# Kernel tuning notes

Hardware: AMD Instinct MI355X
Metric: run time of the kernel (lower is better)

Reference implementation:

```python
import jax, jax.numpy as jnp
import numpy as np

NEG_INF = -1e9


def setup_inputs() -> dict:
    key = jax.random.key(0)
    ks = jax.random.split(key, 9)
    B, T, E, D, H = 64, 2048, 1024, 1024, 1024
    enc = jax.random.normal(ks[0], (B, T, E), dtype=jnp.float32)
    dec = jax.random.normal(ks[1], (B, D), dtype=jnp.float32)
    inp_mask = jax.random.randint(ks[2], (B, T), 0, 2, dtype=jnp.int32)
    s = 1.0 / np.sqrt(H)
    W_enc = jax.random.normal(ks[3], (E, H), dtype=jnp.float32) * s
    b_enc = jax.random.normal(ks[4], (H,), dtype=jnp.float32) * 0.01
    W_dec = jax.random.normal(ks[5], (D, H), dtype=jnp.float32) * s
    b_dec = jax.random.normal(ks[6], (H,), dtype=jnp.float32) * 0.01
    W_out = jax.random.normal(ks[7], (H, 1), dtype=jnp.float32) * s
    b_out = jax.random.normal(ks[8], (1,), dtype=jnp.float32) * 0.01
    return {"enc": enc, "dec": dec, "inp_mask": inp_mask,
            "W_enc": W_enc, "b_enc": b_enc, "W_dec": W_dec, "b_dec": b_dec,
            "W_out": W_out, "b_out": b_out}


def reference(enc, dec, inp_mask, W_enc, b_enc, W_dec, b_dec, W_out, b_out):
    # a: [B, T, H] = Linear(enc) + Linear(dec)[:, None, :]
    a = jnp.einsum('bte,eh->bth', enc, W_enc) + b_enc \
        + (dec @ W_dec + b_dec)[:, None, :]
    a = jnp.tanh(a)
    # scores: [B, T]
    scores = (jnp.einsum('bth,h->bt', a, W_out[:, 0]) + b_out[0])
    scores = jnp.where(inp_mask == 0, NEG_INF, scores)
    probs = jax.nn.softmax(scores, axis=1)            # [B, T]
    attn = jnp.einsum('bt,bte->be', probs, enc)       # [B, E]
    return (attn, probs)
```

## Files before the change

### kernel.cpp

```cpp
#include <hip/hip_runtime.h>
#include <hip/hip_bf16.h>

typedef __attribute__((ext_vector_type(4))) float f32x4;
typedef __attribute__((ext_vector_type(4))) unsigned int u32x4;
typedef __attribute__((ext_vector_type(8))) short s16x8;

static constexpr int Bb = 64;
static constexpr int Tt = 2048;
static constexpr int Ee = 1024;
static constexpr int Hh = 1024;
static constexpr int ATTN_N = Bb * Ee;
static constexpr int PROB_N = Bb * Tt;

__device__ inline unsigned short f2bf(float f) {
    __hip_bfloat16 h = __float2bfloat16(f);
    return __builtin_bit_cast(unsigned short, h);
}

__device__ inline void gload_lds16(const unsigned short* g, unsigned short* l) {
    __builtin_amdgcn_global_load_lds(
        (const __attribute__((address_space(1))) void*)g,
        (__attribute__((address_space(3))) void*)l,
        16, 0, 0);
}

__global__ void wtrans_kernel(const float* __restrict__ w_enc,
                              unsigned short* __restrict__ w16t) {
    __shared__ float tile[32][33];
    const int bx = blockIdx.x & 31;
    const int by = blockIdx.x >> 5;
    const int tx = threadIdx.x & 31;
    const int ty = threadIdx.x >> 5;
#pragma unroll
    for (int j = 0; j < 4; ++j) {
        int e = by * 32 + ty + j * 8;
        int h = bx * 32 + tx;
        tile[ty + j * 8][tx] = w_enc[e * Hh + h];
    }
    __syncthreads();
#pragma unroll
    for (int j = 0; j < 4; ++j) {
        int h = bx * 32 + ty + j * 8;
        int e = by * 32 + tx;
        w16t[h * Ee + e] = f2bf(tile[tx][ty + j * 8]);
    }
}

__global__ void ddec_kernel(const float* __restrict__ dec,
                            const float* __restrict__ w_dec,
                            const float* __restrict__ b_dec,
                            const float* __restrict__ b_enc,
                            float* __restrict__ ddec) {
    const int b = blockIdx.y;
    const int h = blockIdx.x * 256 + threadIdx.x;
    float acc = b_dec[h] + b_enc[h];
    const float* dr = dec + b * Ee;
#pragma unroll 4
    for (int e = 0; e < Ee; ++e) {
        acc += dr[e] * w_dec[e * Hh + h];
    }
    ddec[b * Hh + h] = acc;
}

__global__ __launch_bounds__(512, 2) void gemm_score_kernel(
    const float* __restrict__ enc, const unsigned short* __restrict__ w16t,
    const float* __restrict__ ddec, const float* __restrict__ w_out,
    float* __restrict__ scores) {
    __shared__ unsigned short As[2][256 * 32];
    __shared__ unsigned short Bs[2][256 * 32];

    const int tid = threadIdx.x;
    const int lane = tid & 63;
    const int wid = tid >> 6;
    const int wm = wid >> 2;
    const int wn = wid & 3;
    const int lr = lane & 15;
    const int lg = lane >> 4;

    const int g = blockIdx.x;
    const int xcd = g & 7;
    const int slot = g >> 3;
    const int ntile = slot & 3;
    const int mtile = xcd * 64 + (slot >> 2);
    const int m0 = mtile * 256;
    const int n0 = ntile * 256;
    const int bidx = m0 >> 11;

    const int ar = tid >> 2;
    const int as = tid & 3;

    f32x4 rs[4];

    auto loadA = [&](int kt) {
        const float* src = enc + (size_t)(m0 + ar) * Ee + kt * 32 + as * 8;
#pragma unroll
        for (int ci = 0; ci < 2; ++ci) {
            rs[ci * 2]     = *reinterpret_cast<const f32x4*>(src + (size_t)(128 * ci) * Ee);
            rs[ci * 2 + 1] = *reinterpret_cast<const f32x4*>(src + (size_t)(128 * ci) * Ee + 4);
        }
    };
    auto writeA = [&](int db) {
        char* abase = (char*)&As[db][0];
#pragma unroll
        for (int ci = 0; ci < 2; ++ci) {
            int r = ar + 128 * ci;
            int xr = (r & 3) ^ ((r >> 2) & 1);
            u32x4 w;
            w.x = (unsigned)f2bf(rs[2 * ci].x) | ((unsigned)f2bf(rs[2 * ci].y) << 16);
            w.y = (unsigned)f2bf(rs[2 * ci].z) | ((unsigned)f2bf(rs[2 * ci].w) << 16);
            w.z = (unsigned)f2bf(rs[2 * ci + 1].x) | ((unsigned)f2bf(rs[2 * ci + 1].y) << 16);
            w.w = (unsigned)f2bf(rs[2 * ci + 1].z) | ((unsigned)f2bf(rs[2 * ci + 1].w) << 16);
            *reinterpret_cast<u32x4*>(abase + r * 64 + ((as ^ xr) << 4)) = w;
        }
    };
    auto stageB = [&](int kt, int db) {
        const int sg = (lane & 3) ^ ((lane >> 2) & 3) ^ ((lane >> 4) & 1);
#pragma unroll
        for (int c = 0; c < 2; ++c) {
            int rr = (wid * 2 + c) * 16 + (lane >> 2);
            const unsigned short* src = w16t + (size_t)(n0 + rr) * Ee + kt * 32 + sg * 8;
            gload_lds16(src, &Bs[db][(wid * 2 + c) * 512]);
        }
    };

    f32x4 acc[8][4];
#pragma unroll
    for (int ni = 0; ni < 4; ++ni) {
        float dv = ddec[bidx * Hh + n0 + wn * 64 + ni * 16 + lr];
#pragma unroll
        for (int mi = 0; mi < 8; ++mi) {
            acc[mi][ni].x = dv; acc[mi][ni].y = dv;
            acc[mi][ni].z = dv; acc[mi][ni].w = dv;
        }
    }

    u32x4 af[4], bf[4];
    auto readB4 = [&](int db) {
        const char* bbase = (const char*)&Bs[db][0];
#pragma unroll
        for (int ni = 0; ni < 4; ++ni) {
            int r = wn * 64 + ni * 16 + lr;
            int xr = (r & 3) ^ ((r >> 2) & 1);
            bf[ni] = *reinterpret_cast<const u32x4*>(
                bbase + r * 64 + ((lg ^ xr) << 4));
        }
    };
    auto readA4 = [&](int db, int mib) {
        const char* abase = (const char*)&As[db][0];
#pragma unroll
        for (int k = 0; k < 4; ++k) {
            int r = wm * 128 + (mib + k) * 16 + lr;
            int xr = (r & 3) ^ ((r >> 2) & 1);
            af[k] = *reinterpret_cast<const u32x4*>(
                abase + r * 64 + ((lg ^ xr) << 4));
        }
    };
    auto mfma16 = [&](int mib) {
        __builtin_amdgcn_s_setprio(1);
#pragma unroll
        for (int k = 0; k < 4; ++k)
#pragma unroll
            for (int ni = 0; ni < 4; ++ni)
                acc[mib + k][ni] = __builtin_amdgcn_mfma_f32_16x16x32_bf16(
                    __builtin_bit_cast(s16x8, af[k]),
                    __builtin_bit_cast(s16x8, bf[ni]),
                    acc[mib + k][ni], 0, 0, 0);
        __builtin_amdgcn_s_setprio(0);
    };

#define LGKM0() asm volatile("s_waitcnt lgkmcnt(0)" ::: "memory")

    loadA(0);
    writeA(0);
    LGKM0();
    stageB(0, 0);
    loadA(1);
    asm volatile("s_waitcnt vmcnt(4)" ::: "memory");
    __builtin_amdgcn_s_barrier();

#pragma unroll 1
    for (int tt = 0; tt < 32; tt += 2) {
#pragma unroll
        for (int pp = 0; pp < 2; ++pp) {
            const int t = tt + pp;
            if (t < 31) stageB(t + 1, pp ^ 1);
            readB4(pp);
            readA4(pp, 0);
            mfma16(0);
            if (t < 31) writeA(pp ^ 1);
            readA4(pp, 4);
            mfma16(4);
            LGKM0();
            if (t < 30) {
                loadA(t + 2);
                asm volatile("s_waitcnt vmcnt(4)" ::: "memory");
            } else if (t == 30) {
                asm volatile("s_waitcnt vmcnt(0)" ::: "memory");
            }
            __builtin_amdgcn_s_barrier();
        }
    }

    float wout[4];
#pragma unroll
    for (int ni = 0; ni < 4; ++ni)
        wout[ni] = w_out[n0 + wn * 64 + ni * 16 + lr];

#pragma unroll
    for (int mi = 0; mi < 8; ++mi) {
#pragma unroll
        for (int i = 0; i < 4; ++i) {
            float s = 0.f;
#pragma unroll
            for (int ni = 0; ni < 4; ++ni) {
                float x = (i == 0) ? acc[mi][ni].x : (i == 1) ? acc[mi][ni].y
                           : (i == 2) ? acc[mi][ni].z : acc[mi][ni].w;
                float t = 1.f - 2.f / (__expf(2.f * x) + 1.f);
                s += t * wout[ni];
            }
            s += __shfl_xor(s, 1);
            s += __shfl_xor(s, 2);
            s += __shfl_xor(s, 4);
            s += __shfl_xor(s, 8);
            if (lr == 0) {
                int row = m0 + wm * 128 + mi * 16 + 4 * lg + i;
                atomicAdd(&scores[row], s);
            }
        }
    }
#undef LGKM0
}

__global__ __launch_bounds__(256) void softmax_kernel(float* __restrict__ sc,
                                                      const int* __restrict__ mask) {
    __shared__ float red[256];
    const int b = blockIdx.x;
    const int tid = threadIdx.x;
    float* row = sc + b * Tt;
    const int* mrow = mask + b * Tt;

    float v[8];
    float mx = -3.0e38f;
#pragma unroll
    for (int j = 0; j < 8; ++j) {
        int t = tid + j * 256;
        float s = row[t];
        v[j] = (mrow[t] == 0) ? -1.0e9f : s;
        mx = fmaxf(mx, v[j]);
    }
    red[tid] = mx;
    __syncthreads();
    for (int off = 128; off > 0; off >>= 1) {
        if (tid < off) red[tid] = fmaxf(red[tid], red[tid + off]);
        __syncthreads();
    }
    mx = red[0];
    __syncthreads();

    float p[8];
    float sum = 0.f;
#pragma unroll
    for (int j = 0; j < 8; ++j) {
        p[j] = __expf(v[j] - mx);
        sum += p[j];
    }
    red[tid] = sum;
    __syncthreads();
    for (int off = 128; off > 0; off >>= 1) {
        if (tid < off) red[tid] += red[tid + off];
        __syncthreads();
    }
    float inv = 1.f / red[0];
#pragma unroll
    for (int j = 0; j < 8; ++j)
        row[tid + j * 256] = p[j] * inv;
}

__global__ __launch_bounds__(256) void attn_kernel(const float* __restrict__ enc,
                                                   const float* __restrict__ probs,
                                                   float* __restrict__ attn) {
    __shared__ float pr[128];
    const int b = blockIdx.y;
    const int tc = blockIdx.x;
    const int tid = threadIdx.x;
    if (tid < 128) pr[tid] = probs[b * Tt + tc * 128 + tid];
    __syncthreads();

    const int e0 = tid * 4;
    f32x4 acc; acc.x = 0.f; acc.y = 0.f; acc.z = 0.f; acc.w = 0.f;
    const float* base = enc + (size_t)b * Tt * Ee + (size_t)tc * 128 * Ee + e0;
#pragma unroll 4
    for (int t = 0; t < 128; ++t) {
        f32x4 vv = *reinterpret_cast<const f32x4*>(base + (size_t)t * Ee);
        float pw = pr[t];
        acc.x += pw * vv.x; acc.y += pw * vv.y;
        acc.z += pw * vv.z; acc.w += pw * vv.w;
    }
    atomicAdd(&attn[b * Ee + e0 + 0], acc.x);
    atomicAdd(&attn[b * Ee + e0 + 1], acc.y);
    atomicAdd(&attn[b * Ee + e0 + 2], acc.z);
    atomicAdd(&attn[b * Ee + e0 + 3], acc.w);
}

extern "C" void kernel_launch(void* const* d_in, const int* in_sizes, int n_in,
                              void* d_out, int out_size, void* d_ws, size_t ws_size,
                              hipStream_t stream) {
    const float* enc      = (const float*)d_in[0];
    const float* dec      = (const float*)d_in[1];
    const int*   inp_mask = (const int*)d_in[2];
    const float* W_enc    = (const float*)d_in[3];
    const float* b_enc    = (const float*)d_in[4];
    const float* W_dec    = (const float*)d_in[5];
    const float* b_dec    = (const float*)d_in[6];
    const float* W_out    = (const float*)d_in[7];

    float* attn   = (float*)d_out;
    float* scores = (float*)d_out + ATTN_N;

    unsigned short* w16t = (unsigned short*)d_ws;
    float* ddec = attn;

    hipMemsetAsync(scores, 0, (size_t)PROB_N * sizeof(float), stream);

    wtrans_kernel<<<dim3(1024), 256, 0, stream>>>(W_enc, w16t);
    ddec_kernel<<<dim3(4, 64), 256, 0, stream>>>(dec, W_dec, b_dec, b_enc, ddec);
    gemm_score_kernel<<<dim3(2048), 512, 0, stream>>>(enc, w16t, ddec, W_out, scores);

    hipMemsetAsync(attn, 0, (size_t)ATTN_N * sizeof(float), stream);

    softmax_kernel<<<dim3(64), 256, 0, stream>>>(scores, inp_mask);
    attn_kernel<<<dim3(16, 64), 256, 0, stream>>>(enc, scores, attn);
}
```

Baseline: 650.8 us.

## Emit bf16 copy of enc from GEMM and read it in attention pass

The GEMM kernel's ntile-0 blocks now also write the bf16-converted enc tile to a workspace buffer. The attention-weighted sum then reads this bf16 copy instead of the fp32 enc, halving that pass's read traffic. In exchange the GEMM takes an extra 256 MB of global writes, the attention output loses precision from bf16 rounding, and the path only runs if the workspace holds 256 MB more.

```diff
diff --git a/kernel.cpp b/kernel.cpp
--- a/kernel.cpp
+++ b/kernel.cpp
@@ -3,6 +3,7 @@
 
 typedef __attribute__((ext_vector_type(4))) float f32x4;
 typedef __attribute__((ext_vector_type(4))) unsigned int u32x4;
+typedef __attribute__((ext_vector_type(2))) unsigned int u32x2;
 typedef __attribute__((ext_vector_type(8))) short s16x8;
 
 static constexpr int Bb = 64;
@@ -15,6 +16,9 @@
 __device__ inline unsigned short f2bf(float f) {
     __hip_bfloat16 h = __float2bfloat16(f);
     return __builtin_bit_cast(unsigned short, h);
+}
+__device__ inline float bf2f(unsigned short u) {
+    return __builtin_bit_cast(float, (unsigned)u << 16);
 }
 
 __device__ inline void gload_lds16(const unsigned short* g, unsigned short* l) {
@@ -65,7 +69,8 @@
 __global__ __launch_bounds__(512, 2) void gemm_score_kernel(
     const float* __restrict__ enc, const unsigned short* __restrict__ w16t,
     const float* __restrict__ ddec, const float* __restrict__ w_out,
-    float* __restrict__ scores) {
+    float* __restrict__ scores, unsigned short* __restrict__ enc16out,
+    int doWrite16) {
     __shared__ unsigned short As[2][256 * 32];
     __shared__ unsigned short Bs[2][256 * 32];
 
@@ -88,6 +93,7 @@
 
     const int ar = tid >> 2;
     const int as = tid & 3;
+    const bool st16 = doWrite16 && (ntile == 0);
 
     f32x4 rs[4];
 
@@ -99,7 +105,7 @@
             rs[ci * 2 + 1] = *reinterpret_cast<const f32x4*>(src + (size_t)(128 * ci) * Ee + 4);
         }
     };
-    auto writeA = [&](int db) {
+    auto writeA = [&](int db, int kt) {
         char* abase = (char*)&As[db][0];
 #pragma unroll
         for (int ci = 0; ci < 2; ++ci) {
@@ -111,6 +117,9 @@
             w.z = (unsigned)f2bf(rs[2 * ci + 1].x) | ((unsigned)f2bf(rs[2 * ci + 1].y) << 16);
             w.w = (unsigned)f2bf(rs[2 * ci + 1].z) | ((unsigned)f2bf(rs[2 * ci + 1].w) << 16);
             *reinterpret_cast<u32x4*>(abase + r * 64 + ((as ^ xr) << 4)) = w;
+            if (st16)
+                *reinterpret_cast<u32x4*>(
+                    enc16out + (size_t)(m0 + r) * Ee + kt * 32 + as * 8) = w;
         }
     };
     auto stageB = [&](int kt, int db) {
@@ -171,7 +180,7 @@
 #define LGKM0() asm volatile("s_waitcnt lgkmcnt(0)" ::: "memory")
 
     loadA(0);
-    writeA(0);
+    writeA(0, 0);
     LGKM0();
     stageB(0, 0);
     loadA(1);
@@ -187,13 +196,17 @@
             readB4(pp);
             readA4(pp, 0);
             mfma16(0);
-            if (t < 31) writeA(pp ^ 1);
+            if (t < 31) writeA(pp ^ 1, t + 1);
             readA4(pp, 4);
             mfma16(4);
             LGKM0();
             if (t < 30) {
                 loadA(t + 2);
-                asm volatile("s_waitcnt vmcnt(4)" ::: "memory");
+                if (st16) {
+                    asm volatile("s_waitcnt vmcnt(6)" ::: "memory");
+                } else {
+                    asm volatile("s_waitcnt vmcnt(4)" ::: "memory");
+                }
             } else if (t == 30) {
                 asm volatile("s_waitcnt vmcnt(0)" ::: "memory");
             }
@@ -302,6 +315,34 @@
     atomicAdd(&attn[b * Ee + e0 + 3], acc.w);
 }
 
+__global__ __launch_bounds__(256) void attn_kernel_bf16(
+    const unsigned short* __restrict__ enc16,
+    const float* __restrict__ probs, float* __restrict__ attn) {
+    __shared__ float pr[128];
+    const int b = blockIdx.y;
+    const int tc = blockIdx.x;
+    const int tid = threadIdx.x;
+    if (tid < 128) pr[tid] = probs[b * Tt + tc * 128 + tid];
+    __syncthreads();
+
+    const int e0 = tid * 4;
+    f32x4 acc; acc.x = 0.f; acc.y = 0.f; acc.z = 0.f; acc.w = 0.f;
+    const unsigned short* base = enc16 + (size_t)b * Tt * Ee + (size_t)tc * 128 * Ee + e0;
+#pragma unroll 4
+    for (int t = 0; t < 128; ++t) {
+        u32x2 w = *reinterpret_cast<const u32x2*>(base + (size_t)t * Ee);
+        float pw = pr[t];
+        acc.x += pw * bf2f((unsigned short)(w.x & 0xffff));
+        acc.y += pw * bf2f((unsigned short)(w.x >> 16));
+        acc.z += pw * bf2f((unsigned short)(w.y & 0xffff));
+        acc.w += pw * bf2f((unsigned short)(w.y >> 16));
+    }
+    atomicAdd(&attn[b * Ee + e0 + 0], acc.x);
+    atomicAdd(&attn[b * Ee + e0 + 1], acc.y);
+    atomicAdd(&attn[b * Ee + e0 + 2], acc.z);
+    atomicAdd(&attn[b * Ee + e0 + 3], acc.w);
+}
+
 extern "C" void kernel_launch(void* const* d_in, const int* in_sizes, int n_in,
                               void* d_out, int out_size, void* d_ws, size_t ws_size,
                               hipStream_t stream) {
@@ -318,16 +359,28 @@
     float* scores = (float*)d_out + ATTN_N;
 
     unsigned short* w16t = (unsigned short*)d_ws;
+    const size_t W16T_BYTES = (size_t)Hh * Ee * 2;
+    const size_t ENC16_BYTES = (size_t)Bb * Tt * Ee * 2;
+    const bool fast = ws_size >= W16T_BYTES + ENC16_BYTES;
+    unsigned short* enc16 = (unsigned short*)((char*)d_ws + W16T_BYTES);
+
     float* ddec = attn;
 
     hipMemsetAsync(scores, 0, (size_t)PROB_N * sizeof(float), stream);
 
     wtrans_kernel<<<dim3(1024), 256, 0, stream>>>(W_enc, w16t);
     ddec_kernel<<<dim3(4, 64), 256, 0, stream>>>(dec, W_dec, b_dec, b_enc, ddec);
-    gemm_score_kernel<<<dim3(2048), 512, 0, stream>>>(enc, w16t, ddec, W_out, scores);
+
+    gemm_score_kernel<<<dim3(2048), 512, 0, stream>>>(
+        enc, w16t, ddec, W_out, scores,
+        fast ? enc16 : (unsigned short*)nullptr, fast ? 1 : 0);
 
     hipMemsetAsync(attn, 0, (size_t)ATTN_N * sizeof(float), stream);
 
     softmax_kernel<<<dim3(64), 256, 0, stream>>>(scores, inp_mask);
-    attn_kernel<<<dim3(16, 64), 256, 0, stream>>>(enc, scores, attn);
-}
+    if (fast) {
+        attn_kernel_bf16<<<dim3(16, 64), 256, 0, stream>>>(enc16, scores, attn);
+    } else {
+        attn_kernel<<<dim3(16, 64), 256, 0, stream>>>(enc, scores, attn);
+    }
+}
```

Measured after the change: 678.9 us. 1.04x slower.
